# Performance work log

Measured on AMD Instinct MI355X. Metric: run time of the kernel, lower is better.

Reference implementation:

```python
import jax, jax.numpy as jnp
import numpy as np

N = 100000   # nodes
E = 1600000  # edges (avg degree 16)
N_IN, N_HID, N_OUT = 64, 64, 16


def setup_inputs() -> dict:
    key = jax.random.key(0)
    k1, k2, k3, k4 = jax.random.split(key, 4)
    x = jax.random.normal(k1, (N, N_IN), dtype=jnp.float32)
    edge_index = jax.random.randint(k2, (2, E), 0, N, dtype=jnp.int64)
    # Glorot-style init like PyG GCNConv linear weights
    W1 = jax.random.normal(k3, (N_IN, N_HID), dtype=jnp.float32) * (1.0 / np.sqrt(N_IN))
    b1 = jnp.zeros((N_HID,), dtype=jnp.float32)
    W2 = jax.random.normal(k4, (N_HID, N_OUT), dtype=jnp.float32) * (1.0 / np.sqrt(N_HID))
    b2 = jnp.zeros((N_OUT,), dtype=jnp.float32)
    return {"x": x, "edge_index": edge_index, "W1": W1, "b1": b1, "W2": W2, "b2": b2}


def reference(x, edge_index, W1, b1, W2, b2):
    n = x.shape[0]
    # GCNConv default: add self-loops with weight 1, symmetric normalization
    loop = jnp.arange(n, dtype=edge_index.dtype)
    src = jnp.concatenate([edge_index[0], loop])  # [E+N]
    dst = jnp.concatenate([edge_index[1], loop])  # [E+N]
    w = jnp.ones(src.shape[0], dtype=x.dtype)
    deg = jax.ops.segment_sum(w, dst, num_segments=n)           # in-degree incl. self-loop
    dinv = jnp.where(deg > 0, jax.lax.rsqrt(deg), 0.0)
    norm = dinv[src] * w * dinv[dst]                            # [E+N] edge coefficients

    def gcn_conv(h, Wm, bm):
        h = h @ Wm                                              # [N, d_out] linear first (PyG order)
        msg = h[src] * norm[:, None]                            # gather + scale
        return jax.ops.segment_sum(msg, dst, num_segments=n) + bm  # scatter-add + bias

    h = jax.nn.relu(gcn_conv(x, W1, b1))
    # dropout is identity at inference (training=False)
    return jax.nn.log_softmax(gcn_conv(h, W2, b2), axis=1)
```

## Files before the change

### kernel.cpp

```cpp
#include <hip/hip_runtime.h>

constexpr int FIN = 64;
constexpr int FH  = 64;
constexpr int FO  = 16;


constexpr int BSH      = 7;
constexpr int BW       = 1 << BSH;
constexpr int NBUCK    = 1024;
constexpr int EPB_HIST = 16384;
constexpr int EPB_BIN  = 4096;

constexpr int XT_STRIDE = 68;

__device__ inline unsigned short f2bf(float f) {
    unsigned u = __float_as_uint(f);
    return (unsigned short)((u + 0x7FFFu + ((u >> 16) & 1u)) >> 16);
}
__device__ inline float bf2f(unsigned short h) {
    return __uint_as_float((unsigned)h << 16);
}
__device__ inline float4 bf4_to_f4(ushort4 u) {
    float4 f;
    f.x = bf2f(u.x); f.y = bf2f(u.y); f.z = bf2f(u.z); f.w = bf2f(u.w);
    return f;
}

__launch_bounds__(256)
__global__ void hist_kernel(const int* __restrict__ ei, int E, int* __restrict__ bcnt) {
    __shared__ int lh[NBUCK];
    int t = threadIdx.x;
    for (int i = t; i < NBUCK; i += 256) lh[i] = 0;
    __syncthreads();
    int base = blockIdx.x * EPB_HIST;
    int lim  = min(E, base + EPB_HIST);
    for (int e = base + t; e < lim; e += 256)
        atomicAdd(&lh[ei[E + e] >> BSH], 1);
    __syncthreads();
    for (int b = t; b < NBUCK; b += 256) {
        int c = lh[b];
        if (c > 0) atomicAdd(&bcnt[b], c);
    }
}

__launch_bounds__(1024)
__global__ void bucket_scan_kernel(const int* __restrict__ bcnt, int* __restrict__ bbase,
                                   int* __restrict__ gcur, int* __restrict__ offs,
                                   int N, int E) {
    __shared__ int s[NBUCK];
    int t = threadIdx.x;
    int v = bcnt[t];
    s[t] = v;
    __syncthreads();
    for (int d = 1; d < NBUCK; d <<= 1) {
        int u = (t >= d) ? s[t - d] : 0;
        __syncthreads();
        s[t] += u;
        __syncthreads();
    }
    int ex = s[t] - v;
    bbase[t] = ex;
    gcur[t]  = ex;
    if (t == NBUCK - 1) {
        bbase[NBUCK] = s[t];
        offs[N] = E;
    }
}

__device__ inline void binning_body(const int* __restrict__ ei, int E, int chunk,
                                    int* __restrict__ gcur, unsigned* __restrict__ ebuf,
                                    int* lh) {
    int t = threadIdx.x;
    for (int i = t; i < NBUCK; i += 256) lh[i] = 0;
    __syncthreads();
    int base = chunk * EPB_BIN;
    int lim  = min(E, base + EPB_BIN);
    for (int e = base + t; e < lim; e += 256)
        atomicAdd(&lh[ei[E + e] >> BSH], 1);
    __syncthreads();
    for (int b = t; b < NBUCK; b += 256) {
        int c = lh[b];
        lh[b] = (c > 0) ? atomicAdd(&gcur[b], c) : 0;
    }
    __syncthreads();
    for (int e = base + t; e < lim; e += 256) {
        int d = ei[E + e];
        int srcv = ei[e];
        int pos = atomicAdd(&lh[d >> BSH], 1);
        ebuf[pos] = (unsigned)srcv | ((unsigned)(d & (BW - 1)) << 17);
    }
}

__launch_bounds__(256)
__global__ void binning_kernel(const int* __restrict__ ei, int E,
                               int* __restrict__ gcur, unsigned* __restrict__ ebuf) {
    __shared__ int lh[NBUCK];
    binning_body(ei, E, blockIdx.x, gcur, ebuf, lh);
}

__launch_bounds__(256)
__global__ void gemm1_binning_kernel(const float* __restrict__ x, const float* __restrict__ W1,
                                     unsigned short* __restrict__ hsb,
                                     const int* __restrict__ ei, int E,
                                     int* __restrict__ gcur, unsigned* __restrict__ ebuf,
                                     int N, int G1T) {
    __shared__ float smem[FIN * FH + 64 * XT_STRIDE];
    int tid = threadIdx.x;
    if ((int)blockIdx.x >= G1T) {
        binning_body(ei, E, (int)blockIdx.x - G1T, gcur, ebuf, (int*)smem);
        return;
    }
    float* Ws  = smem;
    float* xsT = smem + FIN * FH;
    {
        const float4* W14 = (const float4*)W1;
        float4* Ws4 = (float4*)Ws;
        for (int i = tid; i < 1024; i += 256) Ws4[i] = W14[i];
    }
    int rowBase = blockIdx.x * 64;
    const float4* x4 = (const float4*)x;
    #pragma unroll
    for (int p = 0; p < 4; ++p) {
        int f   = tid + p * 256;
        int row = f >> 4;
        int c4  = f & 15;
        int grow = rowBase + row;
        float4 v = (grow < N) ? x4[(size_t)grow * 16 + c4]
                              : make_float4(0.f, 0.f, 0.f, 0.f);
        xsT[(c4 * 4 + 0) * XT_STRIDE + row] = v.x;
        xsT[(c4 * 4 + 1) * XT_STRIDE + row] = v.y;
        xsT[(c4 * 4 + 2) * XT_STRIDE + row] = v.z;
        xsT[(c4 * 4 + 3) * XT_STRIDE + row] = v.w;
    }
    __syncthreads();
    int cg = tid & 15;
    int rg = tid >> 4;
    float4 a0 = {0,0,0,0}, a1 = {0,0,0,0}, a2 = {0,0,0,0}, a3 = {0,0,0,0};
    #pragma unroll 8
    for (int k = 0; k < FIN; ++k) {
        float4 wv = *(const float4*)&Ws[k * FH + cg * 4];
        float4 xv = *(const float4*)&xsT[k * XT_STRIDE + rg * 4];
        a0.x = fmaf(xv.x, wv.x, a0.x); a0.y = fmaf(xv.x, wv.y, a0.y);
        a0.z = fmaf(xv.x, wv.z, a0.z); a0.w = fmaf(xv.x, wv.w, a0.w);
        a1.x = fmaf(xv.y, wv.x, a1.x); a1.y = fmaf(xv.y, wv.y, a1.y);
        a1.z = fmaf(xv.y, wv.z, a1.z); a1.w = fmaf(xv.y, wv.w, a1.w);
        a2.x = fmaf(xv.z, wv.x, a2.x); a2.y = fmaf(xv.z, wv.y, a2.y);
        a2.z = fmaf(xv.z, wv.z, a2.z); a2.w = fmaf(xv.z, wv.w, a2.w);
        a3.x = fmaf(xv.w, wv.x, a3.x); a3.y = fmaf(xv.w, wv.y, a3.y);
        a3.z = fmaf(xv.w, wv.z, a3.z); a3.w = fmaf(xv.w, wv.w, a3.w);
    }
    ushort4* hsb4 = (ushort4*)hsb;
    {
        int grow = rowBase + rg * 4 + 0;
        if (grow < N) hsb4[(size_t)grow * 16 + cg] =
            make_ushort4(f2bf(a0.x), f2bf(a0.y), f2bf(a0.z), f2bf(a0.w));
        grow = rowBase + rg * 4 + 1;
        if (grow < N) hsb4[(size_t)grow * 16 + cg] =
            make_ushort4(f2bf(a1.x), f2bf(a1.y), f2bf(a1.z), f2bf(a1.w));
        grow = rowBase + rg * 4 + 2;
        if (grow < N) hsb4[(size_t)grow * 16 + cg] =
            make_ushort4(f2bf(a2.x), f2bf(a2.y), f2bf(a2.z), f2bf(a2.w));
        grow = rowBase + rg * 4 + 3;
        if (grow < N) hsb4[(size_t)grow * 16 + cg] =
            make_ushort4(f2bf(a3.x), f2bf(a3.y), f2bf(a3.z), f2bf(a3.w));
    }
}

__launch_bounds__(256)
__global__ void bucket_csr_kernel(const unsigned* __restrict__ ebuf,
                                  const int* __restrict__ bbase,
                                  int* __restrict__ csr, int* __restrict__ offs,
                                  float* __restrict__ dinv, int N) {
    __shared__ int cnt[BW], sc[BW], cur[BW];
    int t = threadIdx.x;
    int b = blockIdx.x;
    if (t < BW) cnt[t] = 0;
    __syncthreads();
    int beg = bbase[b], end = bbase[b + 1];
    for (int i = beg + t; i < end; i += 256)
        atomicAdd(&cnt[ebuf[i] >> 17], 1);
    __syncthreads();
    if (t < BW) sc[t] = cnt[t];
    __syncthreads();
    for (int d = 1; d < BW; d <<= 1) {
        int u = (t < BW && t >= d) ? sc[t - d] : 0;
        __syncthreads();
        if (t < BW) sc[t] += u;
        __syncthreads();
    }
    int nodeBase = b << BSH;
    if (t < BW) {
        int node = nodeBase + t;
        int ex = beg + sc[t] - cnt[t];
        cur[t] = ex;
        if (node < N) {
            offs[node] = ex;
            dinv[node] = rsqrtf((float)(cnt[t] + 1));
        }
    }
    __syncthreads();
    for (int i = beg + t; i < end; i += 256) {
        unsigned w = ebuf[i];
        int pos = atomicAdd(&cur[w >> 17], 1);
        csr[pos] = (int)(w & 0x1FFFF);
    }
}

__launch_bounds__(256)
__global__ void agg1_gemm2_kernel(const unsigned short* __restrict__ hsb,
                                  const int* __restrict__ csr,
                                  const int* __restrict__ offs, const float* __restrict__ dinv,
                                  const float* __restrict__ b1, const float* __restrict__ W2,
                                  unsigned short* __restrict__ hs2b, int N) {
    __shared__ float W2s[FH * FO];
    __shared__ float h1s[16][68];
    const ushort4* hs4 = (const ushort4*)hsb;
    int tid = threadIdx.x;
    for (int i = tid; i < FH * FO; i += 256) W2s[i] = W2[i];
    int g = tid >> 4, l = tid & 15;
    int n = blockIdx.x * 16 + g;
    if (n < N) {
        float di_n = dinv[n];
        float4 self = bf4_to_f4(hs4[(size_t)n * 16 + l]);
        float4 acc;
        acc.x = self.x * di_n; acc.y = self.y * di_n;
        acc.z = self.z * di_n; acc.w = self.w * di_n;
        int j = offs[n], end = offs[n + 1];
        for (; j + 3 < end; j += 4) {
            int s0 = csr[j], s1 = csr[j + 1], s2 = csr[j + 2], s3 = csr[j + 3];
            float d0 = dinv[s0], d1 = dinv[s1], d2 = dinv[s2], d3 = dinv[s3];
            float4 a = bf4_to_f4(hs4[(size_t)s0 * 16 + l]);
            float4 b = bf4_to_f4(hs4[(size_t)s1 * 16 + l]);
            float4 c = bf4_to_f4(hs4[(size_t)s2 * 16 + l]);
            float4 d = bf4_to_f4(hs4[(size_t)s3 * 16 + l]);
            acc.x = fmaf(a.x, d0, fmaf(b.x, d1, fmaf(c.x, d2, fmaf(d.x, d3, acc.x))));
            acc.y = fmaf(a.y, d0, fmaf(b.y, d1, fmaf(c.y, d2, fmaf(d.y, d3, acc.y))));
            acc.z = fmaf(a.z, d0, fmaf(b.z, d1, fmaf(c.z, d2, fmaf(d.z, d3, acc.z))));
            acc.w = fmaf(a.w, d0, fmaf(b.w, d1, fmaf(c.w, d2, fmaf(d.w, d3, acc.w))));
        }
        for (; j < end; ++j) {
            int s0 = csr[j];
            float d0 = dinv[s0];
            float4 a = bf4_to_f4(hs4[(size_t)s0 * 16 + l]);
            acc.x = fmaf(a.x, d0, acc.x); acc.y = fmaf(a.y, d0, acc.y);
            acc.z = fmaf(a.z, d0, acc.z); acc.w = fmaf(a.w, d0, acc.w);
        }
        float4 bb = ((const float4*)b1)[l];
        float4 h;
        h.x = fmaxf(fmaf(di_n, acc.x, bb.x), 0.f);
        h.y = fmaxf(fmaf(di_n, acc.y, bb.y), 0.f);
        h.z = fmaxf(fmaf(di_n, acc.z, bb.z), 0.f);
        h.w = fmaxf(fmaf(di_n, acc.w, bb.w), 0.f);
        *((float4*)&h1s[g][l * 4]) = h;
    }
    __syncthreads();
    int r = tid >> 4, o = tid & 15;
    int n2 = blockIdx.x * 16 + r;
    if (n2 < N) {
        float acc = 0.f;
        #pragma unroll
        for (int jj = 0; jj < FH; ++jj)
            acc = fmaf(h1s[r][jj], W2s[jj * FO + o], acc);
        hs2b[(size_t)n2 * FO + o] = f2bf(acc * dinv[n2]);
    }
}

__launch_bounds__(256)
__global__ void agg2_softmax_kernel(const unsigned short* __restrict__ hs2b,
                                    const int* __restrict__ csr,
                                    const int* __restrict__ offs, const float* __restrict__ dinv,
                                    const float* __restrict__ b2, float* __restrict__ out, int N) {
    int tid = threadIdx.x;
    int g = tid >> 4, o = tid & 15;
    int n = blockIdx.x * 16 + g;
    float v = 0.f;
    if (n < N) {
        float acc = bf2f(hs2b[(size_t)n * 16 + o]);
        int j = offs[n], end = offs[n + 1];
        for (; j + 3 < end; j += 4) {
            int s0 = csr[j], s1 = csr[j + 1], s2 = csr[j + 2], s3 = csr[j + 3];
            acc += (bf2f(hs2b[(size_t)s0 * 16 + o]) + bf2f(hs2b[(size_t)s1 * 16 + o]))
                 + (bf2f(hs2b[(size_t)s2 * 16 + o]) + bf2f(hs2b[(size_t)s3 * 16 + o]));
        }
        for (; j < end; ++j) acc += bf2f(hs2b[(size_t)csr[j] * 16 + o]);
        v = fmaf(dinv[n], acc, b2[o]);
    }
    float m = v;
    #pragma unroll
    for (int s = 8; s >= 1; s >>= 1) m = fmaxf(m, __shfl_xor(m, s, 64));
    float ex = __expf(v - m);
    float sum = ex;
    #pragma unroll
    for (int s = 8; s >= 1; s >>= 1) sum += __shfl_xor(sum, s, 64);
    if (n < N) out[(size_t)n * FO + o] = v - m - __logf(sum);
}

extern "C" void kernel_launch(void* const* d_in, const int* in_sizes, int n_in,
                              void* d_out, int out_size, void* d_ws, size_t ws_size,
                              hipStream_t stream) {
    const float* x  = (const float*)d_in[0];
    const int*   ei = (const int*)d_in[1];
    const float* W1 = (const float*)d_in[2];
    const float* b1 = (const float*)d_in[3];
    const float* W2 = (const float*)d_in[4];
    const float* b2 = (const float*)d_in[5];
    float* out = (float*)d_out;

    const int N = in_sizes[0] / FIN;
    const int E = in_sizes[1] / 2;
    const int NCH  = (E + EPB_HIST - 1) / EPB_HIST;
    const int NCB  = (E + EPB_BIN - 1) / EPB_BIN;
    const int NB4  = (N + BW - 1) / BW;
    const int G1T  = (N + 63) / 64;
    const int GA   = (N + 15) / 16;

    char* ws = (char*)d_ws;
    size_t off = 0;
    auto alloc = [&](size_t bytes) -> void* {
        off = (off + 255) & ~(size_t)255;
        void* p = ws + off;
        off += bytes;
        return p;
    };
    float*          dinv  = (float*)alloc((size_t)N * 4);
    unsigned short* hsb   = (unsigned short*)alloc((size_t)N * FH * 2);
    unsigned short* hs2b  = (unsigned short*)alloc((size_t)N * FO * 2);
    int*            offs  = (int*)alloc((size_t)(N + 1) * 4);
    int*            bcnt  = (int*)alloc(NBUCK * 4);
    int*            bbase = (int*)alloc((NBUCK + 1) * 4);
    int*            gcur  = (int*)alloc(NBUCK * 4);
    unsigned* ebuf;
    int*      csr;
    bool ws_fits = (ws_size >= off + 512 + (size_t)E * 8);
    if (ws_fits) {
        ebuf = (unsigned*)alloc((size_t)E * 4);
        csr  = (int*)     alloc((size_t)E * 4);
    } else {
        ebuf = (unsigned*)x;
        csr  = (int*)x + E;
    }

    hipMemsetAsync(bcnt, 0, NBUCK * 4, stream);

    hist_kernel<<<NCH, 256, 0, stream>>>(ei, E, bcnt);
    bucket_scan_kernel<<<1, NBUCK, 0, stream>>>(bcnt, bbase, gcur, offs, N, E);
    if (ws_fits) {
        gemm1_binning_kernel<<<G1T + NCB, 256, 0, stream>>>(x, W1, hsb, ei, E,
                                                            gcur, ebuf, N, G1T);
    } else {
        gemm1_binning_kernel<<<G1T, 256, 0, stream>>>(x, W1, hsb, ei, E,
                                                      gcur, ebuf, N, G1T);
        binning_kernel<<<NCB, 256, 0, stream>>>(ei, E, gcur, ebuf);
    }
    bucket_csr_kernel<<<NB4, 256, 0, stream>>>(ebuf, bbase, csr, offs, dinv, N);
    agg1_gemm2_kernel<<<GA, 256, 0, stream>>>(hsb, csr, offs, dinv, b1, W2, hs2b, N);
    agg2_softmax_kernel<<<GA, 256, 0, stream>>>(hs2b, csr, offs, dinv, b2, out, N);
}
```

Measured before the change: 213.7 us.

## Read x directly into registers in GEMM1, put binning blocks first, unroll gathers 8-wide

The GEMM1 part of the fused kernel no longer stages a transposed x tile in shared memory. Each thread now loads its four rows of x straight from global memory with a software-prefetched float4 stream, which cuts LDS usage and may raise occupancy. The fused launch now places the binning blocks ahead of the GEMM blocks so the longer binning work is scheduled first. Both aggregation kernels unroll the neighbour gather to 8 edges to keep more loads in flight, at the cost of more registers and a changed summation order.

Result: slower. 239.9 us (+12.2%).

```diff
diff --git a/kernel.cpp b/kernel.cpp
--- a/kernel.cpp
+++ b/kernel.cpp
@@ -10,8 +10,6 @@
 constexpr int NBUCK    = 1024;
 constexpr int EPB_HIST = 16384;
 constexpr int EPB_BIN  = 4096;
-
-constexpr int XT_STRIDE = 68;
 
 __device__ inline unsigned short f2bf(float f) {
     unsigned u = __float_as_uint(f);
@@ -103,67 +101,66 @@
                                      unsigned short* __restrict__ hsb,
                                      const int* __restrict__ ei, int E,
                                      int* __restrict__ gcur, unsigned* __restrict__ ebuf,
-                                     int N, int G1T) {
-    __shared__ float smem[FIN * FH + 64 * XT_STRIDE];
+                                     int N, int NBIN) {
+    __shared__ float smem[FIN * FH];
     int tid = threadIdx.x;
-    if ((int)blockIdx.x >= G1T) {
-        binning_body(ei, E, (int)blockIdx.x - G1T, gcur, ebuf, (int*)smem);
+    if ((int)blockIdx.x < NBIN) {
+        binning_body(ei, E, (int)blockIdx.x, gcur, ebuf, (int*)smem);
         return;
     }
-    float* Ws  = smem;
-    float* xsT = smem + FIN * FH;
+    float* Ws = smem;
     {
         const float4* W14 = (const float4*)W1;
-        float4* Ws4 = (float4*)Ws;
+        float4* Ws4 = (float4*)smem;
         for (int i = tid; i < 1024; i += 256) Ws4[i] = W14[i];
-    }
-    int rowBase = blockIdx.x * 64;
-    const float4* x4 = (const float4*)x;
-    #pragma unroll
-    for (int p = 0; p < 4; ++p) {
-        int f   = tid + p * 256;
-        int row = f >> 4;
-        int c4  = f & 15;
-        int grow = rowBase + row;
-        float4 v = (grow < N) ? x4[(size_t)grow * 16 + c4]
-                              : make_float4(0.f, 0.f, 0.f, 0.f);
-        xsT[(c4 * 4 + 0) * XT_STRIDE + row] = v.x;
-        xsT[(c4 * 4 + 1) * XT_STRIDE + row] = v.y;
-        xsT[(c4 * 4 + 2) * XT_STRIDE + row] = v.z;
-        xsT[(c4 * 4 + 3) * XT_STRIDE + row] = v.w;
     }
     __syncthreads();
     int cg = tid & 15;
     int rg = tid >> 4;
-    float4 a0 = {0,0,0,0}, a1 = {0,0,0,0}, a2 = {0,0,0,0}, a3 = {0,0,0,0};
-    #pragma unroll 8
-    for (int k = 0; k < FIN; ++k) {
-        float4 wv = *(const float4*)&Ws[k * FH + cg * 4];
-        float4 xv = *(const float4*)&xsT[k * XT_STRIDE + rg * 4];
-        a0.x = fmaf(xv.x, wv.x, a0.x); a0.y = fmaf(xv.x, wv.y, a0.y);
-        a0.z = fmaf(xv.x, wv.z, a0.z); a0.w = fmaf(xv.x, wv.w, a0.w);
-        a1.x = fmaf(xv.y, wv.x, a1.x); a1.y = fmaf(xv.y, wv.y, a1.y);
-        a1.z = fmaf(xv.y, wv.z, a1.z); a1.w = fmaf(xv.y, wv.w, a1.w);
-        a2.x = fmaf(xv.z, wv.x, a2.x); a2.y = fmaf(xv.z, wv.y, a2.y);
-        a2.z = fmaf(xv.z, wv.z, a2.z); a2.w = fmaf(xv.z, wv.w, a2.w);
-        a3.x = fmaf(xv.w, wv.x, a3.x); a3.y = fmaf(xv.w, wv.y, a3.y);
-        a3.z = fmaf(xv.w, wv.z, a3.z); a3.w = fmaf(xv.w, wv.w, a3.w);
+    int rowBase = ((int)blockIdx.x - NBIN) * 64;
+    int r0 = rowBase + rg * 4;
+    const float4* x4 = (const float4*)x;
+    size_t ra = (size_t)min(r0 + 0, N - 1) * 16;
+    size_t rb = (size_t)min(r0 + 1, N - 1) * 16;
+    size_t rc = (size_t)min(r0 + 2, N - 1) * 16;
+    size_t rd = (size_t)min(r0 + 3, N - 1) * 16;
+    float4 acc0 = {0,0,0,0}, acc1 = {0,0,0,0}, acc2 = {0,0,0,0}, acc3 = {0,0,0,0};
+    float4 xa0 = x4[ra], xa1 = x4[rb], xa2 = x4[rc], xa3 = x4[rd];
+    #pragma unroll
+    for (int kc = 0; kc < 16; ++kc) {
+        float4 xb0, xb1, xb2, xb3;
+        if (kc < 15) {
+            xb0 = x4[ra + kc + 1]; xb1 = x4[rb + kc + 1];
+            xb2 = x4[rc + kc + 1]; xb3 = x4[rd + kc + 1];
+        }
+        const float* xa0f = (const float*)&xa0;
+        const float* xa1f = (const float*)&xa1;
+        const float* xa2f = (const float*)&xa2;
+        const float* xa3f = (const float*)&xa3;
+        #pragma unroll
+        for (int j = 0; j < 4; ++j) {
+            float4 wv = *(const float4*)&Ws[(kc * 4 + j) * FH + cg * 4];
+            float v0 = xa0f[j], v1 = xa1f[j], v2 = xa2f[j], v3 = xa3f[j];
+            acc0.x = fmaf(v0, wv.x, acc0.x); acc0.y = fmaf(v0, wv.y, acc0.y);
+            acc0.z = fmaf(v0, wv.z, acc0.z); acc0.w = fmaf(v0, wv.w, acc0.w);
+            acc1.x = fmaf(v1, wv.x, acc1.x); acc1.y = fmaf(v1, wv.y, acc1.y);
+            acc1.z = fmaf(v1, wv.z, acc1.z); acc1.w = fmaf(v1, wv.w, acc1.w);
+            acc2.x = fmaf(v2, wv.x, acc2.x); acc2.y = fmaf(v2, wv.y, acc2.y);
+            acc2.z = fmaf(v2, wv.z, acc2.z); acc2.w = fmaf(v2, wv.w, acc2.w);
+            acc3.x = fmaf(v3, wv.x, acc3.x); acc3.y = fmaf(v3, wv.y, acc3.y);
+            acc3.z = fmaf(v3, wv.z, acc3.z); acc3.w = fmaf(v3, wv.w, acc3.w);
+        }
+        xa0 = xb0; xa1 = xb1; xa2 = xb2; xa3 = xb3;
     }
     ushort4* hsb4 = (ushort4*)hsb;
-    {
-        int grow = rowBase + rg * 4 + 0;
-        if (grow < N) hsb4[(size_t)grow * 16 + cg] =
-            make_ushort4(f2bf(a0.x), f2bf(a0.y), f2bf(a0.z), f2bf(a0.w));
-        grow = rowBase + rg * 4 + 1;
-        if (grow < N) hsb4[(size_t)grow * 16 + cg] =
-            make_ushort4(f2bf(a1.x), f2bf(a1.y), f2bf(a1.z), f2bf(a1.w));
-        grow = rowBase + rg * 4 + 2;
-        if (grow < N) hsb4[(size_t)grow * 16 + cg] =
-            make_ushort4(f2bf(a2.x), f2bf(a2.y), f2bf(a2.z), f2bf(a2.w));
-        grow = rowBase + rg * 4 + 3;
-        if (grow < N) hsb4[(size_t)grow * 16 + cg] =
-            make_ushort4(f2bf(a3.x), f2bf(a3.y), f2bf(a3.z), f2bf(a3.w));
-    }
+    if (r0 + 0 < N) hsb4[(size_t)(r0 + 0) * 16 + cg] =
+        make_ushort4(f2bf(acc0.x), f2bf(acc0.y), f2bf(acc0.z), f2bf(acc0.w));
+    if (r0 + 1 < N) hsb4[(size_t)(r0 + 1) * 16 + cg] =
+        make_ushort4(f2bf(acc1.x), f2bf(acc1.y), f2bf(acc1.z), f2bf(acc1.w));
+    if (r0 + 2 < N) hsb4[(size_t)(r0 + 2) * 16 + cg] =
+        make_ushort4(f2bf(acc2.x), f2bf(acc2.y), f2bf(acc2.z), f2bf(acc2.w));
+    if (r0 + 3 < N) hsb4[(size_t)(r0 + 3) * 16 + cg] =
+        make_ushort4(f2bf(acc3.x), f2bf(acc3.y), f2bf(acc3.z), f2bf(acc3.w));
 }
 
 __launch_bounds__(256)
@@ -226,24 +223,44 @@
         acc.x = self.x * di_n; acc.y = self.y * di_n;
         acc.z = self.z * di_n; acc.w = self.w * di_n;
         int j = offs[n], end = offs[n + 1];
-        for (; j + 3 < end; j += 4) {
-            int s0 = csr[j], s1 = csr[j + 1], s2 = csr[j + 2], s3 = csr[j + 3];
+        for (; j + 7 < end; j += 8) {
+            int s0 = csr[j],     s1 = csr[j + 1], s2 = csr[j + 2], s3 = csr[j + 3];
+            int s4 = csr[j + 4], s5 = csr[j + 5], s6 = csr[j + 6], s7 = csr[j + 7];
             float d0 = dinv[s0], d1 = dinv[s1], d2 = dinv[s2], d3 = dinv[s3];
-            float4 a = bf4_to_f4(hs4[(size_t)s0 * 16 + l]);
-            float4 b = bf4_to_f4(hs4[(size_t)s1 * 16 + l]);
-            float4 c = bf4_to_f4(hs4[(size_t)s2 * 16 + l]);
-            float4 d = bf4_to_f4(hs4[(size_t)s3 * 16 + l]);
-            acc.x = fmaf(a.x, d0, fmaf(b.x, d1, fmaf(c.x, d2, fmaf(d.x, d3, acc.x))));
-            acc.y = fmaf(a.y, d0, fmaf(b.y, d1, fmaf(c.y, d2, fmaf(d.y, d3, acc.y))));
-            acc.z = fmaf(a.z, d0, fmaf(b.z, d1, fmaf(c.z, d2, fmaf(d.z, d3, acc.z))));
-            acc.w = fmaf(a.w, d0, fmaf(b.w, d1, fmaf(c.w, d2, fmaf(d.w, d3, acc.w))));
-        }
-        for (; j < end; ++j) {
+            float d4 = dinv[s4], d5 = dinv[s5], d6 = dinv[s6], d7 = dinv[s7];
+            float4 a0 = bf4_to_f4(hs4[(size_t)s0 * 16 + l]);
+            float4 a1 = bf4_to_f4(hs4[(size_t)s1 * 16 + l]);
+            float4 a2 = bf4_to_f4(hs4[(size_t)s2 * 16 + l]);
+            float4 a3 = bf4_to_f4(hs4[(size_t)s3 * 16 + l]);
+            float4 a4 = bf4_to_f4(hs4[(size_t)s4 * 16 + l]);
+            float4 a5 = bf4_to_f4(hs4[(size_t)s5 * 16 + l]);
+            float4 a6 = bf4_to_f4(hs4[(size_t)s6 * 16 + l]);
+            float4 a7 = bf4_to_f4(hs4[(size_t)s7 * 16 + l]);
+            acc.x += (fmaf(a0.x, d0, a1.x * d1) + fmaf(a2.x, d2, a3.x * d3))
+                   + (fmaf(a4.x, d4, a5.x * d5) + fmaf(a6.x, d6, a7.x * d7));
+            acc.y += (fmaf(a0.y, d0, a1.y * d1) + fmaf(a2.y, d2, a3.y * d3))
+                   + (fmaf(a4.y, d4, a5.y * d5) + fmaf(a6.y, d6, a7.y * d7));
+            acc.z += (fmaf(a0.z, d0, a1.z * d1) + fmaf(a2.z, d2, a3.z * d3))
+                   + (fmaf(a4.z, d4, a5.z * d5) + fmaf(a6.z, d6, a7.z * d7));
+            acc.w += (fmaf(a0.w, d0, a1.w * d1) + fmaf(a2.w, d2, a3.w * d3))
+                   + (fmaf(a4.w, d4, a5.w * d5) + fmaf(a6.w, d6, a7.w * d7));
+        }
+        for (; j + 1 < end; j += 2) {
+            int s0 = csr[j], s1 = csr[j + 1];
+            float d0 = dinv[s0], d1 = dinv[s1];
+            float4 a0 = bf4_to_f4(hs4[(size_t)s0 * 16 + l]);
+            float4 a1 = bf4_to_f4(hs4[(size_t)s1 * 16 + l]);
+            acc.x += fmaf(a0.x, d0, a1.x * d1);
+            acc.y += fmaf(a0.y, d0, a1.y * d1);
+            acc.z += fmaf(a0.z, d0, a1.z * d1);
+            acc.w += fmaf(a0.w, d0, a1.w * d1);
+        }
+        if (j < end) {
             int s0 = csr[j];
             float d0 = dinv[s0];
-            float4 a = bf4_to_f4(hs4[(size_t)s0 * 16 + l]);
-            acc.x = fmaf(a.x, d0, acc.x); acc.y = fmaf(a.y, d0, acc.y);
-            acc.z = fmaf(a.z, d0, acc.z); acc.w = fmaf(a.w, d0, acc.w);
+            float4 a0 = bf4_to_f4(hs4[(size_t)s0 * 16 + l]);
+            acc.x = fmaf(a0.x, d0, acc.x); acc.y = fmaf(a0.y, d0, acc.y);
+            acc.z = fmaf(a0.z, d0, acc.z); acc.w = fmaf(a0.w, d0, acc.w);
         }
         float4 bb = ((const float4*)b1)[l];
         float4 h;
@@ -277,10 +294,14 @@
     if (n < N) {
         float acc = bf2f(hs2b[(size_t)n * 16 + o]);
         int j = offs[n], end = offs[n + 1];
-        for (; j + 3 < end; j += 4) {
-            int s0 = csr[j], s1 = csr[j + 1], s2 = csr[j + 2], s3 = csr[j + 3];
-            acc += (bf2f(hs2b[(size_t)s0 * 16 + o]) + bf2f(hs2b[(size_t)s1 * 16 + o]))
-                 + (bf2f(hs2b[(size_t)s2 * 16 + o]) + bf2f(hs2b[(size_t)s3 * 16 + o]));
+        for (; j + 7 < end; j += 8) {
+            int s0 = csr[j],     s1 = csr[j + 1], s2 = csr[j + 2], s3 = csr[j + 3];
+            int s4 = csr[j + 4], s5 = csr[j + 5], s6 = csr[j + 6], s7 = csr[j + 7];
+            float t0 = bf2f(hs2b[(size_t)s0 * 16 + o]) + bf2f(hs2b[(size_t)s1 * 16 + o]);
+            float t1 = bf2f(hs2b[(size_t)s2 * 16 + o]) + bf2f(hs2b[(size_t)s3 * 16 + o]);
+            float t2 = bf2f(hs2b[(size_t)s4 * 16 + o]) + bf2f(hs2b[(size_t)s5 * 16 + o]);
+            float t3 = bf2f(hs2b[(size_t)s6 * 16 + o]) + bf2f(hs2b[(size_t)s7 * 16 + o]);
+            acc += (t0 + t1) + (t2 + t3);
         }
         for (; j < end; ++j) acc += bf2f(hs2b[(size_t)csr[j] * 16 + o]);
         v = fmaf(dinv[n], acc, b2[o]);
@@ -345,11 +366,11 @@
     hist_kernel<<<NCH, 256, 0, stream>>>(ei, E, bcnt);
     bucket_scan_kernel<<<1, NBUCK, 0, stream>>>(bcnt, bbase, gcur, offs, N, E);
     if (ws_fits) {
-        gemm1_binning_kernel<<<G1T + NCB, 256, 0, stream>>>(x, W1, hsb, ei, E,
-                                                            gcur, ebuf, N, G1T);
+        gemm1_binning_kernel<<<NCB + G1T, 256, 0, stream>>>(x, W1, hsb, ei, E,
+                                                            gcur, ebuf, N, NCB);
     } else {
         gemm1_binning_kernel<<<G1T, 256, 0, stream>>>(x, W1, hsb, ei, E,
-                                                      gcur, ebuf, N, G1T);
+                                                      gcur, ebuf, N, 0);
         binning_kernel<<<NCB, 256, 0, stream>>>(ei, E, gcur, ebuf);
     }
     bucket_csr_kernel<<<NB4, 256, 0, stream>>>(ebuf, bbase, csr, offs, dinv, N);
```
